# Kernel optimization log

Hardware: AMD Instinct MI355X
Metric: run time of the kernel (lower is better)

## Reference

```python
import jax, jax.numpy as jnp
import numpy as np

N_NODES = 100000
N_EDGES = 1600000
IN_F = 128
HID = 16
NEG_SLOPE = 0.2


def setup_inputs() -> dict:
    key = jax.random.key(0)
    ks = jax.random.split(key, 12)
    x = jax.random.normal(ks[0], (N_NODES, IN_F), dtype=jnp.float32)
    edge_index = jax.random.randint(ks[1], (2, N_EDGES), 0, N_NODES, dtype=jnp.int32)
    s1 = 1.0 / np.sqrt(IN_F)
    s2 = 1.0 / np.sqrt(2 * HID)
    # layer 1: heads=2, out=16, concat -> 32
    W1 = jax.random.normal(ks[2], (IN_F, 2 * HID), dtype=jnp.float32) * s1
    a_src1 = jax.random.normal(ks[3], (2, HID), dtype=jnp.float32) * s2
    a_dst1 = jax.random.normal(ks[4], (2, HID), dtype=jnp.float32) * s2
    b1 = jnp.zeros((2 * HID,), dtype=jnp.float32)
    # layer 2: heads=1, out=1
    W2 = jax.random.normal(ks[5], (2 * HID, 1), dtype=jnp.float32) * s2
    a_src2 = jax.random.normal(ks[6], (1, 1), dtype=jnp.float32)
    a_dst2 = jax.random.normal(ks[7], (1, 1), dtype=jnp.float32)
    b2 = jnp.zeros((1,), dtype=jnp.float32)
    return {"x": x, "edge_index": edge_index, "W1": W1, "a_src1": a_src1,
            "a_dst1": a_dst1, "b1": b1, "W2": W2, "a_src2": a_src2,
            "a_dst2": a_dst2, "b2": b2}


def gat_conv(x, src, dst, W, a_src, a_dst, bias, heads, out_ch, concat):
    # PyG GATConv: linear proj, per-edge leaky-relu score, segment softmax over
    # incoming edges (dst), scatter-add aggregation. Self loops already in src/dst.
    n = x.shape[0]
    h = (x @ W).reshape(n, heads, out_ch)                      # [N,H,C]
    alpha_s = (h * a_src[None]).sum(-1)                        # [N,H]
    alpha_d = (h * a_dst[None]).sum(-1)                        # [N,H]
    e = jax.nn.leaky_relu(alpha_s[src] + alpha_d[dst], NEG_SLOPE)  # [E,H]
    m = jax.lax.stop_gradient(jax.ops.segment_max(e, dst, num_segments=n))
    ex = jnp.exp(e - m[dst])
    denom = jax.ops.segment_sum(ex, dst, num_segments=n)       # [N,H]
    alpha = ex / (denom[dst] + 1e-16)                          # [E,H]
    out = jax.ops.segment_sum(alpha[..., None] * h[src], dst, num_segments=n)  # [N,H,C]
    out = out.reshape(n, heads * out_ch) if concat else out.mean(axis=1)
    return out + bias


def reference(x, edge_index, W1, a_src1, a_dst1, b1, W2, a_src2, a_dst2, b2):
    n = x.shape[0]
    loop = jnp.arange(n, dtype=edge_index.dtype)
    src = jnp.concatenate([edge_index[0], loop])
    dst = jnp.concatenate([edge_index[1], loop])
    h = jax.nn.elu(gat_conv(x, src, dst, W1, a_src1, a_dst1, b1, 2, HID, True))
    out = gat_conv(h, src, dst, W2, a_src2, a_dst2, b2, 1, 1, False)
    return out
```

## Files before the change

kernel.cpp:

```cpp
#include <hip/hip_runtime.h>
#include <math.h>

#define IN_F 128
#define C1 32
#define NEG 0.2f
#define XPAD 132
#define BSZ 256
#define CAP 4992
#define EPB 8192

typedef _Float16 h16;
typedef _Float16 h16x2 __attribute__((ext_vector_type(2)));
typedef _Float16 h16x4 __attribute__((ext_vector_type(4)));

__device__ __forceinline__ float leaky(float x) { return x >= 0.f ? x : NEG * x; }

__global__ __launch_bounds__(256)
void k_proj1(const float* __restrict__ x, const float* __restrict__ W1,
             const float* __restrict__ a_s, const float* __restrict__ a_d,
             h16* __restrict__ h1h, float* __restrict__ as1,
             float* __restrict__ ad1, int N) {
    __shared__ float Wl[IN_F * C1];
    __shared__ float xs[32][XPAD];
    int t = threadIdx.x;
    for (int i = t; i < IN_F * C1 / 4; i += 256)
        ((float4*)Wl)[i] = ((const float4*)W1)[i];
    int nl = t >> 3, colq = t & 7;
    int node = blockIdx.x * 32 + nl;
    if (node < N) {
        const float4* xr = (const float4*)(x + (size_t)node * IN_F);
        #pragma unroll
        for (int q = 0; q < 4; ++q) {
            int f4 = colq + q * 8;
            *(float4*)&xs[nl][f4 * 4] = xr[f4];
        }
    }
    __syncthreads();
    if (node >= N) return;
    float4 acc = {0.f, 0.f, 0.f, 0.f};
    const float4* wp = (const float4*)Wl;
    #pragma unroll 4
    for (int k4 = 0; k4 < IN_F / 4; ++k4) {
        float4 xv = *(const float4*)&xs[nl][k4 * 4];
        float4 w0 = wp[(k4 * 4 + 0) * 8 + colq];
        float4 w1 = wp[(k4 * 4 + 1) * 8 + colq];
        float4 w2 = wp[(k4 * 4 + 2) * 8 + colq];
        float4 w3 = wp[(k4 * 4 + 3) * 8 + colq];
        acc.x = fmaf(xv.x, w0.x, acc.x); acc.y = fmaf(xv.x, w0.y, acc.y);
        acc.z = fmaf(xv.x, w0.z, acc.z); acc.w = fmaf(xv.x, w0.w, acc.w);
        acc.x = fmaf(xv.y, w1.x, acc.x); acc.y = fmaf(xv.y, w1.y, acc.y);
        acc.z = fmaf(xv.y, w1.z, acc.z); acc.w = fmaf(xv.y, w1.w, acc.w);
        acc.x = fmaf(xv.z, w2.x, acc.x); acc.y = fmaf(xv.z, w2.y, acc.y);
        acc.z = fmaf(xv.z, w2.z, acc.z); acc.w = fmaf(xv.z, w2.w, acc.w);
        acc.x = fmaf(xv.w, w3.x, acc.x); acc.y = fmaf(xv.w, w3.y, acc.y);
        acc.z = fmaf(xv.w, w3.z, acc.z); acc.w = fmaf(xv.w, w3.w, acc.w);
    }
    h16x4 hv = { (h16)acc.x, (h16)acc.y, (h16)acc.z, (h16)acc.w };
    *(h16x4*)(h1h + (size_t)node * C1 + colq * 4) = hv;
    int cb = colq * 4;
    float sv = acc.x * a_s[cb] + acc.y * a_s[cb + 1] + acc.z * a_s[cb + 2] + acc.w * a_s[cb + 3];
    float dv = acc.x * a_d[cb] + acc.y * a_d[cb + 1] + acc.z * a_d[cb + 2] + acc.w * a_d[cb + 3];
    sv += __shfl_xor(sv, 1); dv += __shfl_xor(dv, 1);
    sv += __shfl_xor(sv, 2); dv += __shfl_xor(dv, 2);
    if (colq == 0) { as1[node * 2 + 0] = sv; ad1[node * 2 + 0] = dv; }
    if (colq == 4) { as1[node * 2 + 1] = sv; ad1[node * 2 + 1] = dv; }
}

__global__ __launch_bounds__(256)
void k_mscat(const int* __restrict__ ei, int E, int ET, int nbk,
             int* __restrict__ bcnt, int* __restrict__ ebuf) {
    __shared__ int hist[512];
    __shared__ int lcur[512];
    int t = threadIdx.x;
    hist[t] = 0; hist[t + 256] = 0;
    __syncthreads();
    int i0 = blockIdx.x * EPB, i1 = min(ET, i0 + EPB);
    for (int i = i0 + t; i < i1; i += 256) {
        int d = (i < E) ? ei[E + i] : i - E;
        atomicAdd(&hist[d >> 8], 1);
    }
    __syncthreads();
    for (int b = t; b < nbk; b += 256) {
        int h = hist[b];
        int base = h ? atomicAdd(&bcnt[b], h) : 0;
        lcur[b] = b * CAP + base;
    }
    __syncthreads();
    for (int i = i0 + t; i < i1; i += 256) {
        int s, d;
        if (i < E) { s = ei[i]; d = ei[E + i]; } else { s = d = i - E; }
        int bkt = d >> 8;
        int pos = atomicAdd(&lcur[bkt], 1);
        if (pos < (bkt + 1) * CAP)
            ebuf[pos] = (s << 8) | (d & 255);
    }
}

__global__ __launch_bounds__(512)
void k_bscan(const int* __restrict__ bcnt, int nbk, int* __restrict__ bbase,
             int* __restrict__ off, int N, int ET) {
    __shared__ int sb[512];
    int t = threadIdx.x;
    int v = (t < nbk) ? min(bcnt[t], CAP) : 0;
    sb[t] = v; __syncthreads();
    for (int o = 1; o < 512; o <<= 1) {
        int xv = (t >= o) ? sb[t - o] : 0; __syncthreads();
        sb[t] += xv; __syncthreads();
    }
    if (t < nbk) bbase[t] = sb[t] - v;
    if (t == nbk - 1) bbase[nbk] = sb[t];
    if (t == 0) off[N] = ET;
}

__global__ __launch_bounds__(256)
void k_bcsr(const int* __restrict__ bcnt, const int* __restrict__ bbase,
            const int* __restrict__ ebuf, int N,
            const float* __restrict__ as1, const float* __restrict__ ad1,
            int* __restrict__ off, int2* __restrict__ csr2) {
    __shared__ int deg[256];
    __shared__ int cur[256];
    __shared__ float adl[512];
    int b = blockIdx.x, t = threadIdx.x;
    int cnt = min(bcnt[b], CAP);
    int ebase = b * CAP;
    int fbase = bbase[b];
    int n0 = b * BSZ;
    deg[t] = 0;
    if (n0 + t < N) ((float2*)adl)[t] = ((const float2*)ad1)[n0 + t];
    __syncthreads();
    for (int i = t; i < cnt; i += 256)
        atomicAdd(&deg[ebuf[ebase + i] & 255], 1);
    __syncthreads();
    int v = deg[t];
    __syncthreads();
    for (int o = 1; o < 256; o <<= 1) {
        int xv = (t >= o) ? deg[t - o] : 0; __syncthreads();
        deg[t] += xv; __syncthreads();
    }
    int excl = deg[t] - v;
    if (n0 + t < N) off[n0 + t] = fbase + excl;
    cur[t] = fbase + excl;
    __syncthreads();
    for (int i = t; i < cnt; i += 256) {
        int e = ebuf[ebase + i];
        int dl = e & 255;
        int s = e >> 8;
        float2 asv = ((const float2*)as1)[s];
        float w0 = __expf(leaky(asv.x + adl[dl * 2 + 0]));
        float w1 = __expf(leaky(asv.y + adl[dl * 2 + 1]));
        h16x2 wp = { (h16)w0, (h16)w1 };
        int p = atomicAdd(&cur[dl], 1);
        int2 rec; rec.x = s; rec.y = *(int*)&wp;
        csr2[p] = rec;
    }
}

__global__ __launch_bounds__(256)
void k_l1agg(const int* __restrict__ off, const int2* __restrict__ csr2,
             const h16* __restrict__ h1h, const float* __restrict__ b1,
             const float* __restrict__ W2, float* __restrict__ p2, int N) {
    int t = threadIdx.x;
    int node = blockIdx.x * 32 + (t >> 3);
    if (node >= N) return;
    int l = t & 7;
    int c0 = l * 4;
    int head = l >> 2;
    float den = 0.f, a0 = 0.f, a1 = 0.f, a2 = 0.f, a3 = 0.f;
    int j0 = off[node], j1 = off[node + 1];
    for (int j = j0; j < j1; j += 4) {
        #pragma unroll
        for (int k = 0; k < 4; ++k) {
            int jj = j + k;
            bool valid = jj < j1;
            jj = valid ? jj : j0;
            int2 e = csr2[jj];
            int s = e.x;
            h16x2 wv = *(h16x2*)&e.y;
            float w = valid ? (float)(head ? wv.y : wv.x) : 0.f;
            h16x4 hv = *(const h16x4*)(h1h + ((size_t)s << 5) + c0);
            den += w;
            a0 = fmaf(w, (float)hv.x, a0);
            a1 = fmaf(w, (float)hv.y, a1);
            a2 = fmaf(w, (float)hv.z, a2);
            a3 = fmaf(w, (float)hv.w, a3);
        }
    }
    float inv = 1.f / (den + 1e-16f);
    float o, val = 0.f;
    o = a0 * inv + b1[c0 + 0]; o = o > 0.f ? o : expm1f(o); val = fmaf(o, W2[c0 + 0], val);
    o = a1 * inv + b1[c0 + 1]; o = o > 0.f ? o : expm1f(o); val = fmaf(o, W2[c0 + 1], val);
    o = a2 * inv + b1[c0 + 2]; o = o > 0.f ? o : expm1f(o); val = fmaf(o, W2[c0 + 2], val);
    o = a3 * inv + b1[c0 + 3]; o = o > 0.f ? o : expm1f(o); val = fmaf(o, W2[c0 + 3], val);
    val += __shfl_xor(val, 1); val += __shfl_xor(val, 2); val += __shfl_xor(val, 4);
    if (l == 0) p2[node] = val;
}

__global__ void k_l2(const int* __restrict__ off, const int2* __restrict__ csr2,
                     const float* __restrict__ p2, const float* __restrict__ as2,
                     const float* __restrict__ ad2, const float* __restrict__ b2,
                     float* __restrict__ out, int N) {
    int i = blockIdx.x * blockDim.x + threadIdx.x;
    if (i >= N) return;
    float A = as2[0];
    float Bc = ad2[0] * p2[i];
    float den = 0.f, num = 0.f;
    int j0 = off[i], j1 = off[i + 1];
    for (int j = j0; j < j1; j += 4) {
        #pragma unroll
        for (int k = 0; k < 4; ++k) {
            int jj = j + k;
            bool valid = jj < j1;
            int s = csr2[valid ? jj : j0].x;
            float ps = p2[s];
            float w = valid ? __expf(leaky(fmaf(ps, A, Bc))) : 0.f;
            den += w;
            num = fmaf(w, ps, num);
        }
    }
    out[i] = num / (den + 1e-16f) + b2[0];
}

extern "C" void kernel_launch(void* const* d_in, const int* in_sizes, int n_in,
                              void* d_out, int out_size, void* d_ws, size_t ws_size,
                              hipStream_t stream) {
    const float* x    = (const float*)d_in[0];
    const int*   ei   = (const int*)d_in[1];
    const float* W1   = (const float*)d_in[2];
    const float* a_s1 = (const float*)d_in[3];
    const float* a_d1 = (const float*)d_in[4];
    const float* b1   = (const float*)d_in[5];
    const float* W2   = (const float*)d_in[6];
    const float* a_s2 = (const float*)d_in[7];
    const float* a_d2 = (const float*)d_in[8];
    const float* b2   = (const float*)d_in[9];
    float* out = (float*)d_out;

    const int N  = in_sizes[0] / IN_F;
    const int E  = in_sizes[1] / 2;
    const int ET = E + N;
    const int nbk = (N + BSZ - 1) / BSZ;

    float* w   = (float*)d_ws;
    float* as1 = w; w += (size_t)2 * N;
    float* ad1 = w; w += (size_t)2 * N;
    float* p2  = w; w += (size_t)N;
    h16* h1h   = (h16*)w;
    w += (size_t)16 * N;
    int* iw     = (int*)w;
    int* bcnt   = iw; iw += 512;
    int* bbase  = iw; iw += 513;
    int* off    = iw; iw += (N + 1);
    iw += (iw - (int*)d_ws) & 1;
    int2* csr2  = (int2*)iw; iw += (size_t)2 * ET;
    int* ebuf   = iw; iw += (size_t)nbk * CAP;

    const int B = 256;
    const int nblkA = (ET + EPB - 1) / EPB;

    hipMemsetAsync(bcnt, 0, 512 * sizeof(int), stream);
    k_proj1<<<(N + 31) / 32, B, 0, stream>>>(x, W1, a_s1, a_d1, h1h, as1, ad1, N);
    k_mscat<<<nblkA, B, 0, stream>>>(ei, E, ET, nbk, bcnt, ebuf);
    k_bscan<<<1, 512, 0, stream>>>(bcnt, nbk, bbase, off, N, ET);
    k_bcsr <<<nbk, B, 0, stream>>>(bcnt, bbase, ebuf, N, as1, ad1, off, csr2);
    k_l1agg<<<(N + 31) / 32, B, 0, stream>>>(off, csr2, h1h, b1, W2, p2, N);
    k_l2   <<<(N + B - 1) / B, B, 0, stream>>>(off, csr2, p2, a_s2, a_d2, b2, out, N);
}
```

Baseline: 226.1 us.

## Fuse projection and edge bucketing into one launch, fold scan into CSR build

Merges the layer-1 projection kernel and the edge bucket-scatter kernel into one launch, with blocks split by index so the two independent jobs run concurrently. Each bucket block now caches its edges in shared memory, so the edge list is read from global memory once instead of twice. The separate single-block bucket scan is removed; each CSR block instead sums the preceding bucket counts itself, and edges per block drop to 2048 so the cache fits. This removes two kernel launches and a serial scan, but adds redundant prefix summation and larger shared-memory use, which may lower occupancy for the projection blocks.

```diff
diff --git a/kernel.cpp b/kernel.cpp
--- a/kernel.cpp
+++ b/kernel.cpp
@@ -7,7 +7,7 @@
 #define XPAD 132
 #define BSZ 256
 #define CAP 4992
-#define EPB 8192
+#define EPB 2048
 
 typedef _Float16 h16;
 typedef _Float16 h16x2 __attribute__((ext_vector_type(2)));
@@ -16,118 +16,113 @@
 __device__ __forceinline__ float leaky(float x) { return x >= 0.f ? x : NEG * x; }
 
 __global__ __launch_bounds__(256)
-void k_proj1(const float* __restrict__ x, const float* __restrict__ W1,
-             const float* __restrict__ a_s, const float* __restrict__ a_d,
-             h16* __restrict__ h1h, float* __restrict__ as1,
-             float* __restrict__ ad1, int N) {
-    __shared__ float Wl[IN_F * C1];
-    __shared__ float xs[32][XPAD];
+void k_fat(const float* __restrict__ x, const float* __restrict__ W1,
+           const float* __restrict__ a_s, const float* __restrict__ a_d,
+           h16* __restrict__ h1h, float* __restrict__ as1,
+           float* __restrict__ ad1, int N,
+           const int* __restrict__ ei, int E, int ET, int nbk,
+           int* __restrict__ bcnt, int* __restrict__ ebuf, int nproj) {
+    __shared__ float smem[IN_F * C1 + 32 * XPAD];
     int t = threadIdx.x;
-    for (int i = t; i < IN_F * C1 / 4; i += 256)
-        ((float4*)Wl)[i] = ((const float4*)W1)[i];
-    int nl = t >> 3, colq = t & 7;
-    int node = blockIdx.x * 32 + nl;
-    if (node < N) {
-        const float4* xr = (const float4*)(x + (size_t)node * IN_F);
-        #pragma unroll
-        for (int q = 0; q < 4; ++q) {
-            int f4 = colq + q * 8;
-            *(float4*)&xs[nl][f4 * 4] = xr[f4];
-        }
-    }
-    __syncthreads();
-    if (node >= N) return;
-    float4 acc = {0.f, 0.f, 0.f, 0.f};
-    const float4* wp = (const float4*)Wl;
-    #pragma unroll 4
-    for (int k4 = 0; k4 < IN_F / 4; ++k4) {
-        float4 xv = *(const float4*)&xs[nl][k4 * 4];
-        float4 w0 = wp[(k4 * 4 + 0) * 8 + colq];
-        float4 w1 = wp[(k4 * 4 + 1) * 8 + colq];
-        float4 w2 = wp[(k4 * 4 + 2) * 8 + colq];
-        float4 w3 = wp[(k4 * 4 + 3) * 8 + colq];
-        acc.x = fmaf(xv.x, w0.x, acc.x); acc.y = fmaf(xv.x, w0.y, acc.y);
-        acc.z = fmaf(xv.x, w0.z, acc.z); acc.w = fmaf(xv.x, w0.w, acc.w);
-        acc.x = fmaf(xv.y, w1.x, acc.x); acc.y = fmaf(xv.y, w1.y, acc.y);
-        acc.z = fmaf(xv.y, w1.z, acc.z); acc.w = fmaf(xv.y, w1.w, acc.w);
-        acc.x = fmaf(xv.z, w2.x, acc.x); acc.y = fmaf(xv.z, w2.y, acc.y);
-        acc.z = fmaf(xv.z, w2.z, acc.z); acc.w = fmaf(xv.z, w2.w, acc.w);
-        acc.x = fmaf(xv.w, w3.x, acc.x); acc.y = fmaf(xv.w, w3.y, acc.y);
-        acc.z = fmaf(xv.w, w3.z, acc.z); acc.w = fmaf(xv.w, w3.w, acc.w);
-    }
-    h16x4 hv = { (h16)acc.x, (h16)acc.y, (h16)acc.z, (h16)acc.w };
-    *(h16x4*)(h1h + (size_t)node * C1 + colq * 4) = hv;
-    int cb = colq * 4;
-    float sv = acc.x * a_s[cb] + acc.y * a_s[cb + 1] + acc.z * a_s[cb + 2] + acc.w * a_s[cb + 3];
-    float dv = acc.x * a_d[cb] + acc.y * a_d[cb + 1] + acc.z * a_d[cb + 2] + acc.w * a_d[cb + 3];
-    sv += __shfl_xor(sv, 1); dv += __shfl_xor(dv, 1);
-    sv += __shfl_xor(sv, 2); dv += __shfl_xor(dv, 2);
-    if (colq == 0) { as1[node * 2 + 0] = sv; ad1[node * 2 + 0] = dv; }
-    if (colq == 4) { as1[node * 2 + 1] = sv; ad1[node * 2 + 1] = dv; }
+    if ((int)blockIdx.x < nproj) {
+        float* Wl = smem;
+        float(*xs)[XPAD] = (float(*)[XPAD])(smem + IN_F * C1);
+        for (int i = t; i < IN_F * C1 / 4; i += 256)
+            ((float4*)Wl)[i] = ((const float4*)W1)[i];
+        int nl = t >> 3, colq = t & 7;
+        int node = blockIdx.x * 32 + nl;
+        if (node < N) {
+            const float4* xr = (const float4*)(x + (size_t)node * IN_F);
+            #pragma unroll
+            for (int q = 0; q < 4; ++q) {
+                int f4 = colq + q * 8;
+                *(float4*)&xs[nl][f4 * 4] = xr[f4];
+            }
+        }
+        __syncthreads();
+        if (node >= N) return;
+        float4 acc = {0.f, 0.f, 0.f, 0.f};
+        const float4* wp = (const float4*)Wl;
+        #pragma unroll 4
+        for (int k4 = 0; k4 < IN_F / 4; ++k4) {
+            float4 xv = *(const float4*)&xs[nl][k4 * 4];
+            float4 w0 = wp[(k4 * 4 + 0) * 8 + colq];
+            float4 w1 = wp[(k4 * 4 + 1) * 8 + colq];
+            float4 w2 = wp[(k4 * 4 + 2) * 8 + colq];
+            float4 w3 = wp[(k4 * 4 + 3) * 8 + colq];
+            acc.x = fmaf(xv.x, w0.x, acc.x); acc.y = fmaf(xv.x, w0.y, acc.y);
+            acc.z = fmaf(xv.x, w0.z, acc.z); acc.w = fmaf(xv.x, w0.w, acc.w);
+            acc.x = fmaf(xv.y, w1.x, acc.x); acc.y = fmaf(xv.y, w1.y, acc.y);
+            acc.z = fmaf(xv.y, w1.z, acc.z); acc.w = fmaf(xv.y, w1.w, acc.w);
+            acc.x = fmaf(xv.z, w2.x, acc.x); acc.y = fmaf(xv.z, w2.y, acc.y);
+            acc.z = fmaf(xv.z, w2.z, acc.z); acc.w = fmaf(xv.z, w2.w, acc.w);
+            acc.x = fmaf(xv.w, w3.x, acc.x); acc.y = fmaf(xv.w, w3.y, acc.y);
+            acc.z = fmaf(xv.w, w3.z, acc.z); acc.w = fmaf(xv.w, w3.w, acc.w);
+        }
+        h16x4 hv = { (h16)acc.x, (h16)acc.y, (h16)acc.z, (h16)acc.w };
+        *(h16x4*)(h1h + (size_t)node * C1 + colq * 4) = hv;
+        int cb = colq * 4;
+        float sv = acc.x * a_s[cb] + acc.y * a_s[cb + 1] + acc.z * a_s[cb + 2] + acc.w * a_s[cb + 3];
+        float dv = acc.x * a_d[cb] + acc.y * a_d[cb + 1] + acc.z * a_d[cb + 2] + acc.w * a_d[cb + 3];
+        sv += __shfl_xor(sv, 1); dv += __shfl_xor(dv, 1);
+        sv += __shfl_xor(sv, 2); dv += __shfl_xor(dv, 2);
+        if (colq == 0) { as1[node * 2 + 0] = sv; ad1[node * 2 + 0] = dv; }
+        if (colq == 4) { as1[node * 2 + 1] = sv; ad1[node * 2 + 1] = dv; }
+    } else {
+        int* hist = (int*)smem;
+        int* lcur = hist + 512;
+        int2* ecache = (int2*)(lcur + 512);
+        int bid = blockIdx.x - nproj;
+        hist[t] = 0; hist[t + 256] = 0;
+        __syncthreads();
+        int i0 = bid * EPB, i1 = min(ET, i0 + EPB);
+        for (int i = i0 + t; i < i1; i += 256) {
+            int s, d;
+            if (i < E) { s = ei[i]; d = ei[E + i]; } else { s = d = i - E; }
+            ecache[i - i0] = make_int2(s, d);
+            atomicAdd(&hist[d >> 8], 1);
+        }
+        __syncthreads();
+        for (int b = t; b < nbk; b += 256) {
+            int h = hist[b];
+            int base = h ? atomicAdd(&bcnt[b], h) : 0;
+            lcur[b] = b * CAP + base;
+        }
+        __syncthreads();
+        for (int i = i0 + t; i < i1; i += 256) {
+            int2 e = ecache[i - i0];
+            int bkt = e.y >> 8;
+            int pos = atomicAdd(&lcur[bkt], 1);
+            if (pos < (bkt + 1) * CAP)
+                ebuf[pos] = (e.x << 8) | (e.y & 255);
+        }
+    }
 }
 
 __global__ __launch_bounds__(256)
-void k_mscat(const int* __restrict__ ei, int E, int ET, int nbk,
-             int* __restrict__ bcnt, int* __restrict__ ebuf) {
-    __shared__ int hist[512];
-    __shared__ int lcur[512];
-    int t = threadIdx.x;
-    hist[t] = 0; hist[t + 256] = 0;
-    __syncthreads();
-    int i0 = blockIdx.x * EPB, i1 = min(ET, i0 + EPB);
-    for (int i = i0 + t; i < i1; i += 256) {
-        int d = (i < E) ? ei[E + i] : i - E;
-        atomicAdd(&hist[d >> 8], 1);
-    }
-    __syncthreads();
-    for (int b = t; b < nbk; b += 256) {
-        int h = hist[b];
-        int base = h ? atomicAdd(&bcnt[b], h) : 0;
-        lcur[b] = b * CAP + base;
-    }
-    __syncthreads();
-    for (int i = i0 + t; i < i1; i += 256) {
-        int s, d;
-        if (i < E) { s = ei[i]; d = ei[E + i]; } else { s = d = i - E; }
-        int bkt = d >> 8;
-        int pos = atomicAdd(&lcur[bkt], 1);
-        if (pos < (bkt + 1) * CAP)
-            ebuf[pos] = (s << 8) | (d & 255);
-    }
-}
-
-__global__ __launch_bounds__(512)
-void k_bscan(const int* __restrict__ bcnt, int nbk, int* __restrict__ bbase,
-             int* __restrict__ off, int N, int ET) {
-    __shared__ int sb[512];
-    int t = threadIdx.x;
-    int v = (t < nbk) ? min(bcnt[t], CAP) : 0;
-    sb[t] = v; __syncthreads();
-    for (int o = 1; o < 512; o <<= 1) {
-        int xv = (t >= o) ? sb[t - o] : 0; __syncthreads();
-        sb[t] += xv; __syncthreads();
-    }
-    if (t < nbk) bbase[t] = sb[t] - v;
-    if (t == nbk - 1) bbase[nbk] = sb[t];
-    if (t == 0) off[N] = ET;
-}
-
-__global__ __launch_bounds__(256)
-void k_bcsr(const int* __restrict__ bcnt, const int* __restrict__ bbase,
-            const int* __restrict__ ebuf, int N,
+void k_bcsr(const int* __restrict__ bcnt, const int* __restrict__ ebuf,
+            int N, int nbk, int ET,
             const float* __restrict__ as1, const float* __restrict__ ad1,
             int* __restrict__ off, int2* __restrict__ csr2) {
     __shared__ int deg[256];
     __shared__ int cur[256];
     __shared__ float adl[512];
+    __shared__ int red[4];
     int b = blockIdx.x, t = threadIdx.x;
+    int part = 0;
+    for (int k = t; k < b; k += 256) part += min(bcnt[k], CAP);
+    part += __shfl_xor(part, 1);  part += __shfl_xor(part, 2);
+    part += __shfl_xor(part, 4);  part += __shfl_xor(part, 8);
+    part += __shfl_xor(part, 16); part += __shfl_xor(part, 32);
+    if ((t & 63) == 0) red[t >> 6] = part;
     int cnt = min(bcnt[b], CAP);
     int ebase = b * CAP;
-    int fbase = bbase[b];
     int n0 = b * BSZ;
     deg[t] = 0;
     if (n0 + t < N) ((float2*)adl)[t] = ((const float2*)ad1)[n0 + t];
     __syncthreads();
+    int fbase = red[0] + red[1] + red[2] + red[3];
+    if (b == nbk - 1 && t == 0) off[N] = fbase + cnt;
     for (int i = t; i < cnt; i += 256)
         atomicAdd(&deg[ebuf[ebase + i] & 255], 1);
     __syncthreads();
@@ -248,20 +243,19 @@
     w += (size_t)16 * N;
     int* iw     = (int*)w;
     int* bcnt   = iw; iw += 512;
-    int* bbase  = iw; iw += 513;
     int* off    = iw; iw += (N + 1);
     iw += (iw - (int*)d_ws) & 1;
     int2* csr2  = (int2*)iw; iw += (size_t)2 * ET;
     int* ebuf   = iw; iw += (size_t)nbk * CAP;
 
     const int B = 256;
+    const int nproj = (N + 31) / 32;
     const int nblkA = (ET + EPB - 1) / EPB;
 
     hipMemsetAsync(bcnt, 0, 512 * sizeof(int), stream);
-    k_proj1<<<(N + 31) / 32, B, 0, stream>>>(x, W1, a_s1, a_d1, h1h, as1, ad1, N);
-    k_mscat<<<nblkA, B, 0, stream>>>(ei, E, ET, nbk, bcnt, ebuf);
-    k_bscan<<<1, 512, 0, stream>>>(bcnt, nbk, bbase, off, N, ET);
-    k_bcsr <<<nbk, B, 0, stream>>>(bcnt, bbase, ebuf, N, as1, ad1, off, csr2);
+    k_fat  <<<nproj + nblkA, B, 0, stream>>>(x, W1, a_s1, a_d1, h1h, as1, ad1, N,
+                                             ei, E, ET, nbk, bcnt, ebuf, nproj);
+    k_bcsr <<<nbk, B, 0, stream>>>(bcnt, ebuf, N, nbk, ET, as1, ad1, off, csr2);
     k_l1agg<<<(N + 31) / 32, B, 0, stream>>>(off, csr2, h1h, b1, W2, p2, N);
     k_l2   <<<(N + B - 1) / B, B, 0, stream>>>(off, csr2, p2, a_s2, a_d2, b2, out, N);
 }
```

Result: faster. 211.8 us (-6.3%).
